# Kernel optimization log

Measured on AMD Instinct MI355X. Metric: run time of the kernel, lower is better.

## Reference

```python
import jax, jax.numpy as jnp
import numpy as np

B, S, D = 2, 2048, 1024
H, DK, DV = 16, 64, 64

def setup_inputs() -> dict:
    key = jax.random.key(0)
    ks = jax.random.split(key, 5)
    scale = 1.0 / np.sqrt(D)  # xavier-ish
    return {
        "Q": jax.random.normal(ks[0], (B, S, D), dtype=jnp.float32),
        "attn_mask": jax.random.uniform(ks[1], (B, S), dtype=jnp.float32),
        "W_Q": jax.random.normal(ks[2], (H * DK, D), dtype=jnp.float32) * scale,
        "b_Q": jnp.zeros((H * DK,), dtype=jnp.float32),
        "W_K": jax.random.normal(ks[3], (H * DK, D), dtype=jnp.float32) * scale,
        "b_K": jnp.zeros((H * DK,), dtype=jnp.float32),
        "W_V": jax.random.normal(ks[4], (H * DV, D), dtype=jnp.float32) * scale,
        "b_V": jnp.zeros((H * DV,), dtype=jnp.float32),
    }

def reference(Q, attn_mask, W_Q, b_Q, W_K, b_K, W_V, b_V):
    b, s, _ = Q.shape
    # projections -> [B, H, S, d]
    q = (Q @ W_Q.T + b_Q).reshape(b, s, H, DK).transpose(0, 2, 1, 3)
    k = (Q @ W_K.T + b_K).reshape(b, s, H, DK).transpose(0, 2, 1, 3)
    v = (Q @ W_V.T + b_V).reshape(b, s, H, DV).transpose(0, 2, 1, 3)
    # exp-based attention (NOT stable softmax), multiplicative mask
    scores = jnp.einsum('bhqd,bhkd->bhqk', q, k) / np.sqrt(DK)
    scores = jnp.exp(scores)
    # mask [B, S_key] broadcast over heads and queries -> [B, 1, 1, S]
    scores = scores * attn_mask[:, None, None, :]
    attn = scores / (jnp.sum(scores, axis=-1, keepdims=True) + 1e-8)
    context = jnp.einsum('bhqk,bhkd->bhqd', attn, v)
    # [B, H, S, DV] -> [B, S, H*DV]
    return context.transpose(0, 2, 1, 3).reshape(b, s, H * DV)
```

## Files before the change

### kernel.cpp

```cpp
#include <hip/hip_runtime.h>
#include <hip/hip_bf16.h>
#include <math.h>

#define BATCH  2
#define S_LEN  2048
#define DMODEL 1024
#define NH     16
#define DHEAD  64

typedef __attribute__((ext_vector_type(8))) short bf16x8;
typedef __attribute__((ext_vector_type(4))) float f32x4;

#define MFMA16(a,b,c) __builtin_amdgcn_mfma_f32_16x16x32_bf16((a),(b),(c),0,0,0)

#define QSCALE 0.18033688011110793f
#define EXP2F(x) __builtin_amdgcn_exp2f(x)

__device__ __forceinline__ unsigned int pkbf(float a, float b) {
    __hip_bfloat162 h = __float22bfloat162_rn(make_float2(a, b));
    union { __hip_bfloat162 h; unsigned int u; } v; v.h = h; return v.u;
}
__device__ __forceinline__ void gl2lds16(const void* g, void* l) {
    __builtin_amdgcn_global_load_lds(
        (const __attribute__((address_space(1))) void*)(g),
        (__attribute__((address_space(3))) void*)(l), 16, 0, 0);
}

__global__ __launch_bounds__(256) void cvt_all(
    const float* __restrict__ Q,  const float* __restrict__ WQ,
    const float* __restrict__ WK, const float* __restrict__ WV,
    const float* __restrict__ msk,
    unsigned short* __restrict__ Qbf, unsigned short* __restrict__ Wbf,
    unsigned short* __restrict__ mbf)
{
    int i = blockIdx.x * blockDim.x + threadIdx.x;
    const float* src;
    unsigned short* dst;
    int off;
    if (i < 524288) {
        src = Q; dst = Qbf; off = i;
    } else if (i < 917504) {
        int j = i - 524288;
        int which = j >> 17;
        src = (which == 0) ? WQ : ((which == 1) ? WK : WV);
        dst = Wbf + ((size_t)which << 20);
        off = j & 131071;
    } else {
        int j = i - 917504;
        if (j >= 512) return;
        src = msk; dst = mbf; off = j;
    }
    float4 a = ((const float4*)src)[2*off];
    float4 b = ((const float4*)src)[2*off + 1];
    uint4 o;
    o.x = pkbf(a.x, a.y); o.y = pkbf(a.z, a.w);
    o.z = pkbf(b.x, b.y); o.w = pkbf(b.z, b.w);
    ((uint4*)dst)[off] = o;
}

__global__ __launch_bounds__(256) void proj_mfma(
    const unsigned short* __restrict__ Abf,
    const unsigned short* __restrict__ Wbf,
    const float* __restrict__ bQ, const float* __restrict__ bK,
    const float* __restrict__ bV, const float* __restrict__ mask,
    unsigned short* __restrict__ qw, unsigned short* __restrict__ kw,
    unsigned short* __restrict__ vt)
{
    __shared__ union {
        struct { unsigned short At[128*32]; unsigned short Bt[128*32]; } s;
        unsigned short Ct[128*132];
    } sm;

    const int tid  = threadIdx.x;
    const int lane = tid & 63;
    const int wv   = tid >> 6;
    const int wm   = (wv >> 1) * 64;
    const int wn   = (wv & 1) * 64;
    const int q15  = lane & 15;
    const int quad = lane >> 4;
    const int z    = blockIdx.z;
    const int n0   = blockIdx.x * 128;
    const int m0   = blockIdx.y * 128;

    const unsigned short* Wz = Wbf + (size_t)z * DMODEL * DMODEL;
    const float* bias = (z == 0) ? bQ : ((z == 1) ? bK : bV);

    f32x4 zero4 = {0.f, 0.f, 0.f, 0.f};
    f32x4 acc[4][4];
    #pragma unroll
    for (int i = 0; i < 4; ++i)
        #pragma unroll
        for (int j = 0; j < 4; ++j) acc[i][j] = zero4;

    for (int k0 = 0; k0 < DMODEL; k0 += 32) {
        __syncthreads();
        #pragma unroll
        for (int c = 0; c < 2; ++c) {
            int o   = tid * 16 + c * 4096;
            int row = o >> 6;
            int cb  = o & 63;
            gl2lds16(Abf + (size_t)(m0 + row) * DMODEL + k0 + (cb >> 1),
                     (char*)sm.s.At + o);
            gl2lds16(Wz  + (size_t)(n0 + row) * DMODEL + k0 + (cb >> 1),
                     (char*)sm.s.Bt + o);
        }
        __syncthreads();

        bf16x8 af[4], bf[4];
        #pragma unroll
        for (int i = 0; i < 4; ++i)
            af[i] = *(const bf16x8*)(sm.s.At + (wm + i*16 + q15) * 32 + quad * 8);
        #pragma unroll
        for (int j = 0; j < 4; ++j)
            bf[j] = *(const bf16x8*)(sm.s.Bt + (wn + j*16 + q15) * 32 + quad * 8);

        if (z < 2) {
            #pragma unroll
            for (int i = 0; i < 4; ++i)
                #pragma unroll
                for (int j = 0; j < 4; ++j)
                    acc[i][j] = MFMA16(bf[j], af[i], acc[i][j]);
        } else {
            #pragma unroll
            for (int i = 0; i < 4; ++i)
                #pragma unroll
                for (int j = 0; j < 4; ++j)
                    acc[i][j] = MFMA16(af[i], bf[j], acc[i][j]);
        }
    }

    __syncthreads();

    if (z < 2) {
        const float qs = (z == 0) ? QSCALE : 1.0f;
        #pragma unroll
        for (int i = 0; i < 4; ++i) {
            int ml = wm + i*16 + q15;
            #pragma unroll
            for (int j = 0; j < 4; ++j) {
                int nl = wn + j*16 + quad*4;
                float4 b4 = *(const float4*)(bias + n0 + nl);
                f32x4 v = acc[i][j];
                uint2 u;
                u.x = pkbf((v.x + b4.x)*qs, (v.y + b4.y)*qs);
                u.y = pkbf((v.z + b4.z)*qs, (v.w + b4.w)*qs);
                *(uint2*)&sm.Ct[ml*132 + nl] = u;
            }
        }
    } else {
        #pragma unroll
        for (int i = 0; i < 4; ++i) {
            int ml = wm + i*16 + quad*4;
            int sg = m0 + ml;
            int b2 = sg >> 11, s0g = sg & 2047;
            float4 mk4 = *(const float4*)(mask + (size_t)b2*S_LEN + s0g);
            #pragma unroll
            for (int j = 0; j < 4; ++j) {
                int nl = wn + j*16 + q15;
                float bv = bias[n0 + nl];
                f32x4 v = acc[i][j];
                uint2 u;
                u.x = pkbf((v.x + bv)*mk4.x, (v.y + bv)*mk4.y);
                u.y = pkbf((v.z + bv)*mk4.z, (v.w + bv)*mk4.w);
                *(uint2*)&sm.Ct[nl*132 + ml] = u;
            }
        }
    }
    __syncthreads();

    {
        int row  = tid >> 1;
        int half = (tid & 1) * 64;
        const uint4* src = (const uint4*)&sm.Ct[row*132 + half];
        unsigned short* dst;
        if (z < 2) {
            unsigned short* outp = (z == 0) ? qw : kw;
            int mg = m0 + row;  int b2 = mg >> 11, s = mg & 2047;
            int n  = n0 + half; int hh = n >> 6;
            dst = outp + (((size_t)b2*NH + hh)*S_LEN + s)*DHEAD;
        } else {
            int n  = n0 + row;  int hh = n >> 6, dv = n & 63;
            int b2 = m0 >> 11, s0 = m0 & 2047;
            dst = vt + (((size_t)b2*NH + hh)*DHEAD + dv)*S_LEN + s0 + half;
        }
        #pragma unroll
        for (int c = 0; c < 8; ++c) ((uint4*)dst)[c] = src[c];
    }
}

__global__ __launch_bounds__(256, 2) void attn_mfma(
    const unsigned short* __restrict__ qw, const unsigned short* __restrict__ kw,
    const unsigned short* __restrict__ vt, const unsigned short* __restrict__ mbf,
    float* __restrict__ out)
{
    __shared__ __align__(16) unsigned short Ks[2][64][72];
    __shared__ __align__(16) unsigned short Vs[2][64][72];
    __shared__ __align__(16) unsigned short Ms[2][72];

    const int tid  = threadIdx.x;
    const int lane = tid & 63;
    const int wv   = tid >> 6;
    const int q15  = lane & 15;
    const int quad = lane >> 4;
    const int q0   = blockIdx.x * 128;
    const int h    = blockIdx.y;
    const int b    = blockIdx.z;

    const size_t headoff = ((size_t)b * NH + h) * S_LEN * DHEAD;
    const unsigned short* qb = qw + headoff;
    const unsigned short* kb = kw + headoff;
    const unsigned short* vb = vt + headoff;
    const unsigned short* mb = mbf + (size_t)b * S_LEN;

    bf16x8 qf[2][2];
    #pragma unroll
    for (int qi = 0; qi < 2; ++qi) {
        const unsigned short* qr = qb + (size_t)(q0 + wv*32 + qi*16 + q15)*DHEAD;
        qf[qi][0] = *(const bf16x8*)(qr + quad*8);
        qf[qi][1] = *(const bf16x8*)(qr + 32 + quad*8);
    }

    const int srow = tid >> 3;
    const int scol = (tid & 7) * 8;
    const int prow = ((srow >> 2) & 1) * 16 + ((srow >> 3) & 3) * 4 + (srow & 3);

    f32x4 zero4 = {0.f, 0.f, 0.f, 0.f};
    f32x4 oacc[2][4];
    f32x4 dacc[2];
    #pragma unroll
    for (int qi = 0; qi < 2; ++qi) {
        dacc[qi] = zero4;
        #pragma unroll
        for (int nj = 0; nj < 4; ++nj) oacc[qi][nj] = zero4;
    }

    uint4 kr0, kr1, vr0, vr1, mr = {0,0,0,0};
    kr0 = *(const uint4*)(kb + (size_t)(srow)     *DHEAD + scol);
    kr1 = *(const uint4*)(kb + (size_t)(srow + 32)*DHEAD + scol);
    vr0 = *(const uint4*)(vb + (size_t)(srow)     *S_LEN + scol);
    vr1 = *(const uint4*)(vb + (size_t)(srow + 32)*S_LEN + scol);
    if (tid < 8) mr = *(const uint4*)(mb + tid*8);

    for (int t = 0; t < 32; ++t) {
        const int buf = t & 1;
        const int k0  = t * 64;
        *(uint4*)&Ks[buf][prow][scol]      = kr0;
        *(uint4*)&Ks[buf][prow + 32][scol] = kr1;
        *(uint4*)&Vs[buf][srow][scol]      = vr0;
        *(uint4*)&Vs[buf][srow + 32][scol] = vr1;
        if (tid < 8) *(uint4*)&Ms[buf][tid*8] = mr;
        const int kn = (t < 31) ? k0 + 64 : 0;
        kr0 = *(const uint4*)(kb + (size_t)(kn + srow)     *DHEAD + scol);
        kr1 = *(const uint4*)(kb + (size_t)(kn + srow + 32)*DHEAD + scol);
        vr0 = *(const uint4*)(vb + (size_t)(srow)     *S_LEN + kn + scol);
        vr1 = *(const uint4*)(vb + (size_t)(srow + 32)*S_LEN + kn + scol);
        if (tid < 8) mr = *(const uint4*)(mb + kn + tid*8);
        __syncthreads();

        f32x4 s[2][4];
        #pragma unroll
        for (int ks = 0; ks < 4; ++ks) {
            bf16x8 kf0 = *(const bf16x8*)&Ks[buf][ks*16 + q15][quad*8];
            bf16x8 kf1 = *(const bf16x8*)&Ks[buf][ks*16 + q15][32 + quad*8];
            #pragma unroll
            for (int qi = 0; qi < 2; ++qi) {
                f32x4 a = MFMA16(kf0, qf[qi][0], zero4);
                s[qi][ks] = MFMA16(kf1, qf[qi][1], a);
            }
        }
        bf16x8 pf[2][2];
        #pragma unroll
        for (int qi = 0; qi < 2; ++qi) {
            uint4 u0, u1;
            u0.x = pkbf(EXP2F(s[qi][0][0]), EXP2F(s[qi][0][1]));
            u0.y = pkbf(EXP2F(s[qi][0][2]), EXP2F(s[qi][0][3]));
            u0.z = pkbf(EXP2F(s[qi][1][0]), EXP2F(s[qi][1][1]));
            u0.w = pkbf(EXP2F(s[qi][1][2]), EXP2F(s[qi][1][3]));
            u1.x = pkbf(EXP2F(s[qi][2][0]), EXP2F(s[qi][2][1]));
            u1.y = pkbf(EXP2F(s[qi][2][2]), EXP2F(s[qi][2][3]));
            u1.z = pkbf(EXP2F(s[qi][3][0]), EXP2F(s[qi][3][1]));
            u1.w = pkbf(EXP2F(s[qi][3][2]), EXP2F(s[qi][3][3]));
            union { uint4 u; bf16x8 h; } c0, c1;
            c0.u = u0; c1.u = u1;
            pf[qi][0] = c0.h;
            pf[qi][1] = c1.h;
        }
        bf16x8 mf0 = *(const bf16x8*)&Ms[buf][quad*8];
        bf16x8 mf1 = *(const bf16x8*)&Ms[buf][32 + quad*8];
        #pragma unroll
        for (int qi = 0; qi < 2; ++qi) {
            dacc[qi] = MFMA16(pf[qi][0], mf0, dacc[qi]);
            dacc[qi] = MFMA16(pf[qi][1], mf1, dacc[qi]);
        }
        #pragma unroll
        for (int nj = 0; nj < 4; ++nj) {
            bf16x8 vf0 = *(const bf16x8*)&Vs[buf][nj*16 + q15][quad*8];
            bf16x8 vf1 = *(const bf16x8*)&Vs[buf][nj*16 + q15][32 + quad*8];
            #pragma unroll
            for (int qi = 0; qi < 2; ++qi) {
                oacc[qi][nj] = MFMA16(pf[qi][0], vf0, oacc[qi][nj]);
                oacc[qi][nj] = MFMA16(pf[qi][1], vf1, oacc[qi][nj]);
            }
        }
    }

    #pragma unroll
    for (int qi = 0; qi < 2; ++qi)
        #pragma unroll
        for (int r = 0; r < 4; ++r) {
            float inv = 1.0f / (dacc[qi][r] + 1e-8f);
            size_t row = ((size_t)b*S_LEN + q0 + wv*32 + qi*16 + quad*4 + r)*DMODEL
                       + h*DHEAD;
            #pragma unroll
            for (int nj = 0; nj < 4; ++nj)
                out[row + nj*16 + q15] = oacc[qi][nj][r] * inv;
        }
}

extern "C" void kernel_launch(void* const* d_in, const int* in_sizes, int n_in,
                              void* d_out, int out_size, void* d_ws, size_t ws_size,
                              hipStream_t stream) {
    const float* Q    = (const float*)d_in[0];
    const float* msk  = (const float*)d_in[1];
    const float* W_Q  = (const float*)d_in[2];
    const float* b_Q  = (const float*)d_in[3];
    const float* W_K  = (const float*)d_in[4];
    const float* b_K  = (const float*)d_in[5];
    const float* W_V  = (const float*)d_in[6];
    const float* b_V  = (const float*)d_in[7];
    float* out = (float*)d_out;

    unsigned short* wsu = (unsigned short*)d_ws;
    unsigned short* Qbf = wsu;
    unsigned short* Wbf = Qbf + (size_t)4096*1024;
    unsigned short* qwb = Wbf + (size_t)3*1024*1024;
    unsigned short* kwb = qwb + (size_t)4*1024*1024;
    unsigned short* vtb = kwb + (size_t)4*1024*1024;
    unsigned short* mbf = vtb + (size_t)4*1024*1024;

    cvt_all<<<3586, 256, 0, stream>>>(Q, W_Q, W_K, W_V, msk, Qbf, Wbf, mbf);

    proj_mfma<<<dim3(8, 32, 3), 256, 0, stream>>>(
        Qbf, Wbf, b_Q, b_K, b_V, msk, qwb, kwb, vtb);

    attn_mfma<<<dim3(S_LEN/128, NH, BATCH), 256, 0, stream>>>(
        qwb, kwb, vtb, mbf, out);
}
```

Before: 181.1 us.

## Register-prefetch double-buffer projection GEMM; split attention into 8 waves of 16 rows

The projection GEMM drops direct global-to-LDS loads and the two-barrier loop. It now prefetches the next K-slice into registers and stores it into a double-buffered LDS tile, which cuts one barrier per step and overlaps loads with MFMA. The attention kernel goes from 256 threads with 32 query rows per wave to 512 threads with 16 rows per wave, raising wave count and occupancy at the cost of less K/V fragment reuse per wave. Each thread now loads one K/V row slice instead of two.

```diff
diff --git a/kernel.cpp b/kernel.cpp
--- a/kernel.cpp
+++ b/kernel.cpp
@@ -19,11 +19,6 @@
 __device__ __forceinline__ unsigned int pkbf(float a, float b) {
     __hip_bfloat162 h = __float22bfloat162_rn(make_float2(a, b));
     union { __hip_bfloat162 h; unsigned int u; } v; v.h = h; return v.u;
-}
-__device__ __forceinline__ void gl2lds16(const void* g, void* l) {
-    __builtin_amdgcn_global_load_lds(
-        (const __attribute__((address_space(1))) void*)(g),
-        (__attribute__((address_space(3))) void*)(l), 16, 0, 0);
 }
 
 __global__ __launch_bounds__(256) void cvt_all(
@@ -67,7 +62,7 @@
     unsigned short* __restrict__ vt)
 {
     __shared__ union {
-        struct { unsigned short At[128*32]; unsigned short Bt[128*32]; } s;
+        struct { unsigned short A[2][4096]; unsigned short B[2][4096]; } s;
         unsigned short Ct[128*132];
     } sm;
 
@@ -85,6 +80,9 @@
     const unsigned short* Wz = Wbf + (size_t)z * DMODEL * DMODEL;
     const float* bias = (z == 0) ? bQ : ((z == 1) ? bK : bV);
 
+    const int r0 = tid >> 2,          c0 = (tid & 3) * 8;
+    const int r1 = (tid + 256) >> 2,  c1 = c0;
+
     f32x4 zero4 = {0.f, 0.f, 0.f, 0.f};
     f32x4 acc[4][4];
     #pragma unroll
@@ -92,27 +90,32 @@
         #pragma unroll
         for (int j = 0; j < 4; ++j) acc[i][j] = zero4;
 
-    for (int k0 = 0; k0 < DMODEL; k0 += 32) {
+    uint4 a0, a1, b0, b1;
+    a0 = *(const uint4*)(Abf + (size_t)(m0 + r0) * DMODEL + c0);
+    a1 = *(const uint4*)(Abf + (size_t)(m0 + r1) * DMODEL + c1);
+    b0 = *(const uint4*)(Wz  + (size_t)(n0 + r0) * DMODEL + c0);
+    b1 = *(const uint4*)(Wz  + (size_t)(n0 + r1) * DMODEL + c1);
+
+    for (int t = 0; t < 32; ++t) {
+        const int buf = t & 1;
+        *(uint4*)(sm.s.A[buf] + r0*32 + c0) = a0;
+        *(uint4*)(sm.s.A[buf] + r1*32 + c1) = a1;
+        *(uint4*)(sm.s.B[buf] + r0*32 + c0) = b0;
+        *(uint4*)(sm.s.B[buf] + r1*32 + c1) = b1;
+        const int kn = (t < 31) ? (t + 1) * 32 : 0;
+        a0 = *(const uint4*)(Abf + (size_t)(m0 + r0) * DMODEL + kn + c0);
+        a1 = *(const uint4*)(Abf + (size_t)(m0 + r1) * DMODEL + kn + c1);
+        b0 = *(const uint4*)(Wz  + (size_t)(n0 + r0) * DMODEL + kn + c0);
+        b1 = *(const uint4*)(Wz  + (size_t)(n0 + r1) * DMODEL + kn + c1);
         __syncthreads();
-        #pragma unroll
-        for (int c = 0; c < 2; ++c) {
-            int o   = tid * 16 + c * 4096;
-            int row = o >> 6;
-            int cb  = o & 63;
-            gl2lds16(Abf + (size_t)(m0 + row) * DMODEL + k0 + (cb >> 1),
-                     (char*)sm.s.At + o);
-            gl2lds16(Wz  + (size_t)(n0 + row) * DMODEL + k0 + (cb >> 1),
-                     (char*)sm.s.Bt + o);
-        }
-        __syncthreads();
 
         bf16x8 af[4], bf[4];
         #pragma unroll
         for (int i = 0; i < 4; ++i)
-            af[i] = *(const bf16x8*)(sm.s.At + (wm + i*16 + q15) * 32 + quad * 8);
+            af[i] = *(const bf16x8*)(sm.s.A[buf] + (wm + i*16 + q15) * 32 + quad * 8);
         #pragma unroll
         for (int j = 0; j < 4; ++j)
-            bf[j] = *(const bf16x8*)(sm.s.Bt + (wn + j*16 + q15) * 32 + quad * 8);
+            bf[j] = *(const bf16x8*)(sm.s.B[buf] + (wn + j*16 + q15) * 32 + quad * 8);
 
         if (z < 2) {
             #pragma unroll
@@ -188,7 +191,7 @@
     }
 }
 
-__global__ __launch_bounds__(256, 2) void attn_mfma(
+__global__ __launch_bounds__(512, 4) void attn_mfma(
     const unsigned short* __restrict__ qw, const unsigned short* __restrict__ kw,
     const unsigned short* __restrict__ vt, const unsigned short* __restrict__ mbf,
     float* __restrict__ out)
@@ -212,109 +215,80 @@
     const unsigned short* vb = vt + headoff;
     const unsigned short* mb = mbf + (size_t)b * S_LEN;
 
-    bf16x8 qf[2][2];
-    #pragma unroll
-    for (int qi = 0; qi < 2; ++qi) {
-        const unsigned short* qr = qb + (size_t)(q0 + wv*32 + qi*16 + q15)*DHEAD;
-        qf[qi][0] = *(const bf16x8*)(qr + quad*8);
-        qf[qi][1] = *(const bf16x8*)(qr + 32 + quad*8);
-    }
+    const unsigned short* qr = qb + (size_t)(q0 + wv*16 + q15)*DHEAD;
+    bf16x8 qf0 = *(const bf16x8*)(qr + quad*8);
+    bf16x8 qf1 = *(const bf16x8*)(qr + 32 + quad*8);
 
     const int srow = tid >> 3;
     const int scol = (tid & 7) * 8;
-    const int prow = ((srow >> 2) & 1) * 16 + ((srow >> 3) & 3) * 4 + (srow & 3);
+    const int prow = (srow & 32) + ((srow >> 2) & 1) * 16
+                   + ((srow >> 3) & 3) * 4 + (srow & 3);
 
     f32x4 zero4 = {0.f, 0.f, 0.f, 0.f};
-    f32x4 oacc[2][4];
-    f32x4 dacc[2];
+    f32x4 oacc[4];
+    f32x4 dacc = zero4;
     #pragma unroll
-    for (int qi = 0; qi < 2; ++qi) {
-        dacc[qi] = zero4;
-        #pragma unroll
-        for (int nj = 0; nj < 4; ++nj) oacc[qi][nj] = zero4;
-    }
-
-    uint4 kr0, kr1, vr0, vr1, mr = {0,0,0,0};
-    kr0 = *(const uint4*)(kb + (size_t)(srow)     *DHEAD + scol);
-    kr1 = *(const uint4*)(kb + (size_t)(srow + 32)*DHEAD + scol);
-    vr0 = *(const uint4*)(vb + (size_t)(srow)     *S_LEN + scol);
-    vr1 = *(const uint4*)(vb + (size_t)(srow + 32)*S_LEN + scol);
+    for (int nj = 0; nj < 4; ++nj) oacc[nj] = zero4;
+
+    uint4 kr, vr, mr = {0,0,0,0};
+    kr = *(const uint4*)(kb + (size_t)srow*DHEAD + scol);
+    vr = *(const uint4*)(vb + (size_t)srow*S_LEN + scol);
     if (tid < 8) mr = *(const uint4*)(mb + tid*8);
 
     for (int t = 0; t < 32; ++t) {
         const int buf = t & 1;
         const int k0  = t * 64;
-        *(uint4*)&Ks[buf][prow][scol]      = kr0;
-        *(uint4*)&Ks[buf][prow + 32][scol] = kr1;
-        *(uint4*)&Vs[buf][srow][scol]      = vr0;
-        *(uint4*)&Vs[buf][srow + 32][scol] = vr1;
+        *(uint4*)&Ks[buf][prow][scol] = kr;
+        *(uint4*)&Vs[buf][srow][scol] = vr;
         if (tid < 8) *(uint4*)&Ms[buf][tid*8] = mr;
         const int kn = (t < 31) ? k0 + 64 : 0;
-        kr0 = *(const uint4*)(kb + (size_t)(kn + srow)     *DHEAD + scol);
-        kr1 = *(const uint4*)(kb + (size_t)(kn + srow + 32)*DHEAD + scol);
-        vr0 = *(const uint4*)(vb + (size_t)(srow)     *S_LEN + kn + scol);
-        vr1 = *(const uint4*)(vb + (size_t)(srow + 32)*S_LEN + kn + scol);
+        kr = *(const uint4*)(kb + (size_t)(kn + srow)*DHEAD + scol);
+        vr = *(const uint4*)(vb + (size_t)srow*S_LEN + kn + scol);
         if (tid < 8) mr = *(const uint4*)(mb + kn + tid*8);
         __syncthreads();
 
-        f32x4 s[2][4];
+        f32x4 s[4];
         #pragma unroll
         for (int ks = 0; ks < 4; ++ks) {
             bf16x8 kf0 = *(const bf16x8*)&Ks[buf][ks*16 + q15][quad*8];
             bf16x8 kf1 = *(const bf16x8*)&Ks[buf][ks*16 + q15][32 + quad*8];
-            #pragma unroll
-            for (int qi = 0; qi < 2; ++qi) {
-                f32x4 a = MFMA16(kf0, qf[qi][0], zero4);
-                s[qi][ks] = MFMA16(kf1, qf[qi][1], a);
-            }
-        }
-        bf16x8 pf[2][2];
-        #pragma unroll
-        for (int qi = 0; qi < 2; ++qi) {
-            uint4 u0, u1;
-            u0.x = pkbf(EXP2F(s[qi][0][0]), EXP2F(s[qi][0][1]));
-            u0.y = pkbf(EXP2F(s[qi][0][2]), EXP2F(s[qi][0][3]));
-            u0.z = pkbf(EXP2F(s[qi][1][0]), EXP2F(s[qi][1][1]));
-            u0.w = pkbf(EXP2F(s[qi][1][2]), EXP2F(s[qi][1][3]));
-            u1.x = pkbf(EXP2F(s[qi][2][0]), EXP2F(s[qi][2][1]));
-            u1.y = pkbf(EXP2F(s[qi][2][2]), EXP2F(s[qi][2][3]));
-            u1.z = pkbf(EXP2F(s[qi][3][0]), EXP2F(s[qi][3][1]));
-            u1.w = pkbf(EXP2F(s[qi][3][2]), EXP2F(s[qi][3][3]));
-            union { uint4 u; bf16x8 h; } c0, c1;
-            c0.u = u0; c1.u = u1;
-            pf[qi][0] = c0.h;
-            pf[qi][1] = c1.h;
-        }
+            f32x4 a = MFMA16(kf0, qf0, zero4);
+            s[ks] = MFMA16(kf1, qf1, a);
+        }
+        uint4 u0, u1;
+        u0.x = pkbf(EXP2F(s[0][0]), EXP2F(s[0][1]));
+        u0.y = pkbf(EXP2F(s[0][2]), EXP2F(s[0][3]));
+        u0.z = pkbf(EXP2F(s[1][0]), EXP2F(s[1][1]));
+        u0.w = pkbf(EXP2F(s[1][2]), EXP2F(s[1][3]));
+        u1.x = pkbf(EXP2F(s[2][0]), EXP2F(s[2][1]));
+        u1.y = pkbf(EXP2F(s[2][2]), EXP2F(s[2][3]));
+        u1.z = pkbf(EXP2F(s[3][0]), EXP2F(s[3][1]));
+        u1.w = pkbf(EXP2F(s[3][2]), EXP2F(s[3][3]));
+        union { uint4 u; bf16x8 h; } c0, c1;
+        c0.u = u0; c1.u = u1;
+        bf16x8 pf0 = c0.h;
+        bf16x8 pf1 = c1.h;
         bf16x8 mf0 = *(const bf16x8*)&Ms[buf][quad*8];
         bf16x8 mf1 = *(const bf16x8*)&Ms[buf][32 + quad*8];
-        #pragma unroll
-        for (int qi = 0; qi < 2; ++qi) {
-            dacc[qi] = MFMA16(pf[qi][0], mf0, dacc[qi]);
-            dacc[qi] = MFMA16(pf[qi][1], mf1, dacc[qi]);
-        }
+        dacc = MFMA16(pf0, mf0, dacc);
+        dacc = MFMA16(pf1, mf1, dacc);
         #pragma unroll
         for (int nj = 0; nj < 4; ++nj) {
             bf16x8 vf0 = *(const bf16x8*)&Vs[buf][nj*16 + q15][quad*8];
             bf16x8 vf1 = *(const bf16x8*)&Vs[buf][nj*16 + q15][32 + quad*8];
-            #pragma unroll
-            for (int qi = 0; qi < 2; ++qi) {
-                oacc[qi][nj] = MFMA16(pf[qi][0], vf0, oacc[qi][nj]);
-                oacc[qi][nj] = MFMA16(pf[qi][1], vf1, oacc[qi][nj]);
-            }
+            oacc[nj] = MFMA16(pf0, vf0, oacc[nj]);
+            oacc[nj] = MFMA16(pf1, vf1, oacc[nj]);
         }
     }
 
     #pragma unroll
-    for (int qi = 0; qi < 2; ++qi)
-        #pragma unroll
-        for (int r = 0; r < 4; ++r) {
-            float inv = 1.0f / (dacc[qi][r] + 1e-8f);
-            size_t row = ((size_t)b*S_LEN + q0 + wv*32 + qi*16 + quad*4 + r)*DMODEL
-                       + h*DHEAD;
-            #pragma unroll
-            for (int nj = 0; nj < 4; ++nj)
-                out[row + nj*16 + q15] = oacc[qi][nj][r] * inv;
-        }
+    for (int r = 0; r < 4; ++r) {
+        float inv = 1.0f / (dacc[r] + 1e-8f);
+        size_t row = ((size_t)b*S_LEN + q0 + wv*16 + quad*4 + r)*DMODEL + h*DHEAD;
+        #pragma unroll
+        for (int nj = 0; nj < 4; ++nj)
+            out[row + nj*16 + q15] = oacc[nj][r] * inv;
+    }
 }
 
 extern "C" void kernel_launch(void* const* d_in, const int* in_sizes, int n_in,
@@ -343,6 +317,6 @@
     proj_mfma<<<dim3(8, 32, 3), 256, 0, stream>>>(
         Qbf, Wbf, b_Q, b_K, b_V, msk, qwb, kwb, vtb);
 
-    attn_mfma<<<dim3(S_LEN/128, NH, BATCH), 256, 0, stream>>>(
+    attn_mfma<<<dim3(S_LEN/128, NH, BATCH), 512, 0, stream>>>(
         qwb, kwb, vtb, mbf, out);
 }
```

New measurement: 190.4 us. 1.05x slower.
